# Optimization experiments

Measured on AMD Instinct MI355X. Metric: run time of the kernel, lower is better.

## Reference

```python
import jax, jax.numpy as jnp
import numpy as np

BN_EPS = 1e-5
LRELU_SLOPE = 0.2
EPS = 1e-8
K = 3


def setup_inputs() -> dict:
    key = jax.random.key(0)
    ks = jax.random.split(key, 8)
    B, Cd, Cs, M, S, N = 8, 256, 512, 4096, 1024, 4096
    return {
        "dense_data": jax.random.normal(ks[0], (B, Cd, M), dtype=jnp.float32),
        "dense_idx": jax.random.randint(ks[1], (B, M), 0, N),
        "sparse_data": jax.random.normal(ks[2], (B, Cs, S), dtype=jnp.float32),
        "sparse_idx": jax.random.randint(ks[3], (B, S), 0, N),
        "pcd": jax.random.normal(ks[4], (B, 3, N), dtype=jnp.float32),
        "conv_w": jax.random.normal(ks[5], (Cd, 3 * Cd), dtype=jnp.float32) * (1.0 / np.sqrt(3 * Cd)),
        "bn_gamma": jnp.ones((Cd,), dtype=jnp.float32),
        "bn_beta": jnp.zeros((Cd,), dtype=jnp.float32),
    }


def _knn_interpolate(dense_xyz, sparse_xyz, sparse_feats, k):
    # dense_xyz: [B,3,M], sparse_xyz: [B,3,S], sparse_feats: [B,Cs,S]
    d2 = (
        jnp.sum(dense_xyz**2, axis=1)[:, :, None]
        + jnp.sum(sparse_xyz**2, axis=1)[:, None, :]
        - 2.0 * jnp.einsum("bdm,bds->bms", dense_xyz, sparse_xyz)
    )  # [B,M,S] squared distances
    neg_d, idx = jax.lax.top_k(-d2, k)  # [B,M,K]
    d_nb = -neg_d
    w = 1.0 / (d_nb + EPS)
    w = w / jnp.sum(w, axis=-1, keepdims=True)  # [B,M,K]
    # gather neighbor features: [B,Cs,M,K]
    nb = jnp.take_along_axis(sparse_feats[:, :, None, :], idx[:, None, :, :], axis=3)
    return jnp.sum(nb * w[:, None, :, :], axis=-1)  # [B,Cs,M]


def reference(dense_data, dense_idx, sparse_data, sparse_idx, pcd, conv_w, bn_gamma, bn_beta):
    # gather xyz coords of dense / sparse points: [B,3,M], [B,3,S]
    dense_xyz = jnp.take_along_axis(pcd, dense_idx[:, None, :], axis=2)
    sparse_xyz = jnp.take_along_axis(pcd, sparse_idx[:, None, :], axis=2)
    interp = _knn_interpolate(dense_xyz, sparse_xyz, sparse_data, K)  # [B,Cs,M]
    x = jnp.concatenate([dense_data, interp], axis=1)  # [B,3*Cd,M]
    # 1x1 conv (no bias)
    y = jnp.einsum("oc,bcm->bom", conv_w, x)
    # BatchNorm1d (training mode: batch statistics over B and M, biased var)
    mu = jnp.mean(y, axis=(0, 2), keepdims=True)
    var = jnp.mean((y - mu) ** 2, axis=(0, 2), keepdims=True)
    y = (y - mu) * jax.lax.rsqrt(var + BN_EPS)
    y = y * bn_gamma[None, :, None] + bn_beta[None, :, None]
    # LeakyReLU(0.2)
    y = jnp.where(y >= 0, y, LRELU_SLOPE * y)
    return (y, dense_idx)
```

## Files before the change

kernel.cpp:

```cpp
#include <hip/hip_runtime.h>
#include <float.h>

#define DEVI __device__ __forceinline__

namespace {

constexpr int NB   = 8;
constexpr int CD   = 256;
constexpr int CS   = 512;
constexpr int MM   = 4096;
constexpr int SS   = 1024;
constexpr int NN   = 4096;
constexpr int KTOT = 768;
constexpr int OC   = 256;
constexpr float KEPS  = 1e-8f;
constexpr float BNEPS = 1e-5f;
constexpr float SLOPE = 0.2f;

constexpr size_t OFF_Z    = 0;
constexpr size_t SZ_Z     = (size_t)NB * SS * OC * 4;
constexpr size_t OFF_RAW  = OFF_Z + SZ_Z;
constexpr size_t SZ_RAW   = (size_t)NB * OC * MM * 2;
constexpr size_t OFF_IDX3 = OFF_RAW + SZ_RAW;
constexpr size_t SZ_IDX3  = (size_t)NB * MM * 3 * 4;
constexpr size_t OFF_W3   = OFF_IDX3 + SZ_IDX3;
constexpr size_t OFF_WBF  = OFF_W3 + SZ_IDX3;
constexpr size_t SZ_WBF   = (size_t)OC * KTOT * 2;
constexpr size_t OFF_PS   = OFF_WBF + SZ_WBF;
constexpr size_t SZ_PS    = (size_t)512 * OC * 4;
constexpr size_t OFF_PS2  = OFF_PS + SZ_PS;
constexpr size_t OFF_A    = OFF_PS2 + SZ_PS;
constexpr size_t OFF_B    = OFF_A + 1024;

typedef __attribute__((ext_vector_type(8))) short s16x8;
typedef __attribute__((ext_vector_type(8))) unsigned short u16x8;
typedef __attribute__((ext_vector_type(4))) float f32x4;

DEVI short f2bf(float f) {
  union { float f; unsigned u; } c; c.f = f;
  unsigned r = c.u + 0x7fffu + ((c.u >> 16) & 1u);
  return (short)(r >> 16);
}

DEVI unsigned umin_(unsigned a, unsigned b) { return a < b ? a : b; }
DEVI unsigned umax_(unsigned a, unsigned b) { return a > b ? a : b; }

__global__ __launch_bounds__(256) void k_knn(
    const int* __restrict__ didx, const int* __restrict__ sidx,
    const float* __restrict__ pcd,
    int* __restrict__ idx3, float* __restrict__ w3,
    float* __restrict__ outIdxF,
    const float* __restrict__ convw, short* __restrict__ wbf) {
  __shared__ float4   sxyz[SS];
  __shared__ unsigned pk[4][64][3];

  int blk = blockIdx.x;
  int b   = blk >> 6;
  int m0  = (blk & 63) << 6;
  int tid = threadIdx.x;
  const float* pb = pcd + (size_t)b * 3 * NN;

  for (int i = tid; i < 384; i += 256) {
    int g = blk * 384 + i;
    wbf[g] = f2bf(convw[g]);
  }

  for (int s = tid; s < SS; s += 256) {
    int si = sidx[b * SS + s];
    float x = pb[si], yy = pb[NN + si], z = pb[2 * NN + si];
    sxyz[s] = make_float4(x, yy, z, x * x + yy * yy + z * z);
  }

  int p     = tid & 63;
  int chunk = tid >> 6;
  int m     = m0 + p;
  int di    = didx[b * MM + m];
  float px = pb[di], py = pb[NN + di], pz = pb[2 * NN + di];
  float pp = px * px + py * py + pz * pz;
  float nx = -2.f * px, ny = -2.f * py, nz = -2.f * pz;

  if (chunk == 0) outIdxF[b * MM + m] = (float)di;

  __syncthreads();

  unsigned k0 = 0xFFFFFFFFu, k1 = 0xFFFFFFFFu, k2 = 0xFFFFFFFFu;
  int s0c = chunk << 8;
#pragma unroll 4
  for (int t = 0; t < 256; ++t) {
    int s = s0c + t;
    float4 c = sxyz[s];
    float d = fmaf(nx, c.x, c.w + pp);
    d = fmaf(ny, c.y, d);
    d = fmaf(nz, c.z, d);
    d = fmaxf(d, 0.f);
    unsigned key = (__float_as_uint(d) & 0xFFFFFC00u) | (unsigned)s;
    unsigned e0 = umax_(key, k0); k0 = umin_(key, k0);
    unsigned e1 = umax_(e0, k1);  k1 = umin_(e0, k1);
    k2 = umin_(e1, k2);
  }
  pk[chunk][p][0] = k0; pk[chunk][p][1] = k1; pk[chunk][p][2] = k2;
  __syncthreads();

  if (tid < 64) {
    unsigned g0 = 0xFFFFFFFFu, g1 = 0xFFFFFFFFu, g2 = 0xFFFFFFFFu;
#pragma unroll
    for (int c = 0; c < 4; ++c)
#pragma unroll
      for (int r = 0; r < 3; ++r) {
        unsigned key = pk[c][p][r];
        unsigned e0 = umax_(key, g0); g0 = umin_(key, g0);
        unsigned e1 = umax_(e0, g1);  g1 = umin_(e0, g1);
        g2 = umin_(e1, g2);
      }
    int j0 = g0 & 1023, j1 = g1 & 1023, j2 = g2 & 1023;
    float e0 = __uint_as_float(g0 & 0xFFFFFC00u);
    float e1 = __uint_as_float(g1 & 0xFFFFFC00u);
    float e2 = __uint_as_float(g2 & 0xFFFFFC00u);
    float w0 = 1.f / (e0 + KEPS), w1 = 1.f / (e1 + KEPS), w2 = 1.f / (e2 + KEPS);
    float inv = 1.f / (w0 + w1 + w2);
    int base = (b * MM + m) * 3;
    idx3[base] = j0; idx3[base + 1] = j1; idx3[base + 2] = j2;
    w3[base] = w0 * inv; w3[base + 1] = w1 * inv; w3[base + 2] = w2 * inv;
  }
}

__global__ __launch_bounds__(256) void k_gemmZ(
    const float* __restrict__ sp, const short* __restrict__ wbf,
    float* __restrict__ Z) {
  __shared__ __align__(16) short Wl[256 * 72];
  __shared__ __align__(16) short Sl[32 * 72];

  int blk = blockIdx.x;
  int st = blk & 31, b = blk >> 5;
  int s0 = st * 32;
  int tid = threadIdx.x, wv = tid >> 6, lane = tid & 63;
  int lo = lane & 15, quad = lane >> 4;

  f32x4 acc[4][2] = {};
  for (int k0 = 0; k0 < CS; k0 += 64) {
    __syncthreads();
#pragma unroll
    for (int r = 0; r < 8; ++r) {
      int lin = r * 256 + tid, row = lin >> 3, c8 = lin & 7;
      uint4 v = *(const uint4*)((const unsigned short*)wbf + (size_t)row * KTOT + CD + k0 + c8 * 8);
      *(uint4*)(&Wl[row * 72 + c8 * 8]) = v;
    }
#pragma unroll
    for (int r = 0; r < 2; ++r) {
      int lin = r * 256 + tid, cc = lin >> 3, s4 = lin & 7;
      float4 v = *(const float4*)(sp + (size_t)(b * CS + k0 + cc) * SS + s0 + s4 * 4);
      Sl[(s4 * 4 + 0) * 72 + cc] = f2bf(v.x);
      Sl[(s4 * 4 + 1) * 72 + cc] = f2bf(v.y);
      Sl[(s4 * 4 + 2) * 72 + cc] = f2bf(v.z);
      Sl[(s4 * 4 + 3) * 72 + cc] = f2bf(v.w);
    }
    __syncthreads();
    s16x8 af[2][4], bfr[2][2];
#pragma unroll
    for (int h = 0; h < 2; ++h) {
#pragma unroll
      for (int i = 0; i < 4; ++i)
        af[h][i] = *(const s16x8*)(&Wl[(wv * 64 + i * 16 + lo) * 72 + h * 32 + quad * 8]);
#pragma unroll
      for (int j = 0; j < 2; ++j)
        bfr[h][j] = *(const s16x8*)(&Sl[(j * 16 + lo) * 72 + h * 32 + quad * 8]);
    }
#pragma unroll
    for (int h = 0; h < 2; ++h)
#pragma unroll
      for (int i = 0; i < 4; ++i)
#pragma unroll
        for (int j = 0; j < 2; ++j)
          acc[i][j] = __builtin_amdgcn_mfma_f32_16x16x32_bf16(af[h][i], bfr[h][j], acc[i][j], 0, 0, 0);
  }
#pragma unroll
  for (int i = 0; i < 4; ++i)
#pragma unroll
    for (int j = 0; j < 2; ++j) {
      int s = j * 16 + lo, o = wv * 64 + i * 16 + quad * 4;
      *(f32x4*)(Z + (size_t)(b * SS + s0 + s) * OC + o) = acc[i][j];
    }
}

__global__ __launch_bounds__(256) void k_gemmDC(
    const float* __restrict__ dense, const float* __restrict__ Z,
    const int* __restrict__ idx3, const float* __restrict__ w3,
    const short* __restrict__ wbf, unsigned short* __restrict__ raw,
    float* __restrict__ ps, float* __restrict__ ps2) {
  __shared__ __align__(16) short Wl[256 * 72];
  __shared__ __align__(16) short Xl[64 * 72];
  __shared__ int   mi3[192];
  __shared__ float mw3[192];

  int blk = blockIdx.x;
  int mt = blk & 63, b = blk >> 6, m0 = mt << 6;
  int tid = threadIdx.x, wv = tid >> 6, lane = tid & 63;
  int lo = lane & 15, quad = lane >> 4;

  {
    int base = (b * MM + m0) * 3;
    for (int i = tid; i < 192; i += 256) { mi3[i] = idx3[base + i]; mw3[i] = w3[base + i]; }
  }

  f32x4 acc[4][4] = {};
  for (int k0 = 0; k0 < CD; k0 += 64) {
    __syncthreads();
#pragma unroll
    for (int r = 0; r < 8; ++r) {
      int lin = r * 256 + tid, row = lin >> 3, c8 = lin & 7;
      uint4 v = *(const uint4*)((const unsigned short*)wbf + (size_t)row * KTOT + k0 + c8 * 8);
      *(uint4*)(&Wl[row * 72 + c8 * 8]) = v;
    }
    {
      int kk4 = tid >> 4, m4 = tid & 15;
      float4 v0 = *(const float4*)(dense + (size_t)(b * CD + k0 + kk4 * 4 + 0) * MM + m0 + m4 * 4);
      float4 v1 = *(const float4*)(dense + (size_t)(b * CD + k0 + kk4 * 4 + 1) * MM + m0 + m4 * 4);
      float4 v2 = *(const float4*)(dense + (size_t)(b * CD + k0 + kk4 * 4 + 2) * MM + m0 + m4 * 4);
      float4 v3 = *(const float4*)(dense + (size_t)(b * CD + k0 + kk4 * 4 + 3) * MM + m0 + m4 * 4);
      ushort4 w;
      w.x = (unsigned short)f2bf(v0.x); w.y = (unsigned short)f2bf(v1.x);
      w.z = (unsigned short)f2bf(v2.x); w.w = (unsigned short)f2bf(v3.x);
      *(ushort4*)(&Xl[(m4 * 4 + 0) * 72 + kk4 * 4]) = w;
      w.x = (unsigned short)f2bf(v0.y); w.y = (unsigned short)f2bf(v1.y);
      w.z = (unsigned short)f2bf(v2.y); w.w = (unsigned short)f2bf(v3.y);
      *(ushort4*)(&Xl[(m4 * 4 + 1) * 72 + kk4 * 4]) = w;
      w.x = (unsigned short)f2bf(v0.z); w.y = (unsigned short)f2bf(v1.z);
      w.z = (unsigned short)f2bf(v2.z); w.w = (unsigned short)f2bf(v3.z);
      *(ushort4*)(&Xl[(m4 * 4 + 2) * 72 + kk4 * 4]) = w;
      w.x = (unsigned short)f2bf(v0.w); w.y = (unsigned short)f2bf(v1.w);
      w.z = (unsigned short)f2bf(v2.w); w.w = (unsigned short)f2bf(v3.w);
      *(ushort4*)(&Xl[(m4 * 4 + 3) * 72 + kk4 * 4]) = w;
    }
    __syncthreads();
    s16x8 af[2][4], bfr[2][4];
#pragma unroll
    for (int h = 0; h < 2; ++h) {
#pragma unroll
      for (int i = 0; i < 4; ++i)
        af[h][i] = *(const s16x8*)(&Wl[(wv * 64 + i * 16 + lo) * 72 + h * 32 + quad * 8]);
#pragma unroll
      for (int j = 0; j < 4; ++j)
        bfr[h][j] = *(const s16x8*)(&Xl[(j * 16 + lo) * 72 + h * 32 + quad * 8]);
    }
#pragma unroll
    for (int h = 0; h < 2; ++h)
#pragma unroll
      for (int i = 0; i < 4; ++i)
#pragma unroll
        for (int j = 0; j < 4; ++j)
          acc[i][j] = __builtin_amdgcn_mfma_f32_16x16x32_bf16(af[h][i], bfr[h][j], acc[i][j], 0, 0, 0);
  }

  float* P = (float*)Wl;
  const float* Zb = Z + (size_t)b * SS * OC;
  unsigned short* rb = raw + (size_t)b * OC * MM;
  float ss[4][4] = {}, s2s[4][4] = {};
  __syncthreads();

#pragma unroll
  for (int h = 0; h < 2; ++h) {
#pragma unroll 4
    for (int ml = 0; ml < 32; ++ml) {
      int mg = (h * 32 + ml) * 3;
      float p = mw3[mg + 0] * Zb[(size_t)mi3[mg + 0] * OC + tid]
              + mw3[mg + 1] * Zb[(size_t)mi3[mg + 1] * OC + tid]
              + mw3[mg + 2] * Zb[(size_t)mi3[mg + 2] * OC + tid];
      P[ml * 260 + tid] = p;
    }
    __syncthreads();
#pragma unroll
    for (int i = 0; i < 4; ++i)
#pragma unroll
      for (int jj = 0; jj < 2; ++jj) {
        int j = h * 2 + jj, ml = jj * 16 + lo;
        int o = wv * 64 + i * 16 + quad * 4;
        f32x4 p = *(const f32x4*)(&P[ml * 260 + o]);
        f32x4 v = acc[i][j] + p;
        unsigned short* dst = rb + (size_t)o * MM + m0 + j * 16 + lo;
#pragma unroll
        for (int r = 0; r < 4; ++r) {
          float vv = v[r];
          dst[(size_t)r * MM] = (unsigned short)f2bf(vv);
          ss[i][r] += vv; s2s[i][r] += vv * vv;
        }
      }
    __syncthreads();
  }

#pragma unroll
  for (int i = 0; i < 4; ++i)
#pragma unroll
    for (int r = 0; r < 4; ++r) {
      float a = ss[i][r], q = s2s[i][r];
      for (int off = 1; off < 16; off <<= 1) { a += __shfl_xor(a, off); q += __shfl_xor(q, off); }
      ss[i][r] = a; s2s[i][r] = q;
    }
  if (lo == 0) {
#pragma unroll
    for (int i = 0; i < 4; ++i)
#pragma unroll
      for (int r = 0; r < 4; ++r) {
        int o = wv * 64 + i * 16 + quad * 4 + r;
        ps[(size_t)blk * OC + o]  = ss[i][r];
        ps2[(size_t)blk * OC + o] = s2s[i][r];
      }
  }
}

__global__ void k_finalize(const float* __restrict__ ps, const float* __restrict__ ps2,
                           const float* __restrict__ gamma, const float* __restrict__ beta,
                           float* __restrict__ sA, float* __restrict__ sB) {
  __shared__ float red[512];
  int blk = blockIdx.x;
  int tid = threadIdx.x;
  int ch = tid & 31, sl = tid >> 5;
  int o = blk * 32 + ch;
  float s = 0.f, s2 = 0.f;
#pragma unroll 4
  for (int j = 0; j < 64; ++j) {
    int k = sl * 64 + j;
    s  += ps[(size_t)k * OC + o];
    s2 += ps2[(size_t)k * OC + o];
  }
  red[sl * 32 + ch] = s;
  red[256 + sl * 32 + ch] = s2;
  __syncthreads();
  if (tid < 32) {
    float S = 0.f, S2 = 0.f;
#pragma unroll
    for (int t = 0; t < 8; ++t) { S += red[t * 32 + tid]; S2 += red[256 + t * 32 + tid]; }
    int oo = blk * 32 + tid;
    float mn = S / (float)(NB * MM);
    float vr = S2 / (float)(NB * MM) - mn * mn;
    float a  = rsqrtf(vr + BNEPS) * gamma[oo];
    sA[oo] = a;
    sB[oo] = beta[oo] - mn * a;
  }
}

__global__ void k_norm(const unsigned short* __restrict__ raw, float* __restrict__ y,
                       const float* __restrict__ sA, const float* __restrict__ sB) {
  int i = blockIdx.x * 256 + threadIdx.x;
  int o = (i >> 9) & 255;
  float a = sA[o], be = sB[o];
  u16x8 v = ((const u16x8*)raw)[i];
  float out[8];
#pragma unroll
  for (int r = 0; r < 8; ++r) {
    union { unsigned u; float f; } c; c.u = ((unsigned)v[r]) << 16;
    float t = c.f * a + be;
    out[r] = t >= 0.f ? t : SLOPE * t;
  }
  float4* dst = (float4*)(y + (size_t)i * 8);
  dst[0] = make_float4(out[0], out[1], out[2], out[3]);
  dst[1] = make_float4(out[4], out[5], out[6], out[7]);
}

}

extern "C" void kernel_launch(void* const* d_in, const int* in_sizes, int n_in,
                              void* d_out, int out_size, void* d_ws, size_t ws_size,
                              hipStream_t stream) {
  const float* dense = (const float*)d_in[0];
  const int*   didx  = (const int*)d_in[1];
  const float* sp    = (const float*)d_in[2];
  const int*   sidx  = (const int*)d_in[3];
  const float* pcd   = (const float*)d_in[4];
  const float* convw = (const float*)d_in[5];
  const float* gamma = (const float*)d_in[6];
  const float* beta  = (const float*)d_in[7];

  float* y = (float*)d_out;
  float* outIdxF = y + (size_t)NB * OC * MM;

  char* ws = (char*)d_ws;
  float*          Z    = (float*)(ws + OFF_Z);
  unsigned short* raw  = (unsigned short*)(ws + OFF_RAW);
  int*            idx3 = (int*)(ws + OFF_IDX3);
  float*          w3   = (float*)(ws + OFF_W3);
  short*          wbf  = (short*)(ws + OFF_WBF);
  float*          ps   = (float*)(ws + OFF_PS);
  float*          ps2  = (float*)(ws + OFF_PS2);
  float*          sA   = (float*)(ws + OFF_A);
  float*          sB   = (float*)(ws + OFF_B);

  k_knn     <<<NB * (MM / 64), 256, 0, stream>>>(didx, sidx, pcd, idx3, w3, outIdxF, convw, wbf);
  k_gemmZ   <<<NB * (SS / 32), 256, 0, stream>>>(sp, wbf, Z);
  k_gemmDC  <<<NB * (MM / 64), 256, 0, stream>>>(dense, Z, idx3, w3, wbf, raw, ps, ps2);
  k_finalize<<<8, 256, 0, stream>>>(ps, ps2, gamma, beta, sA, sB);
  k_norm    <<<(NB * OC * MM / 8) / 256, 256, 0, stream>>>(raw, y, sA, sB);
}
```

Measured before the change: 163.3 us.

## Fuse BN finalize into normalize kernel and process two query points per KNN thread

The BN statistics finalize kernel is removed: partial sums are now stored channel-major, and each normalize block (one per batch/channel row) reduces the 512 partials for its channel before applying scale, shift and LeakyReLU. This drops one kernel launch and the tiny 8-block finalize stage, but repeats the channel reduction across all 8 batches. Separately, the KNN kernel now handles 128 query points per block, two per thread. Each shared-memory read of sparse xyz is reused for two distance computations, and half as many blocks reload the sparse coordinates.

Result: no change. 163.9 us (+0.4%).

```diff
diff --git a/kernel.cpp b/kernel.cpp
--- a/kernel.cpp
+++ b/kernel.cpp
@@ -29,8 +29,6 @@
 constexpr size_t OFF_PS   = OFF_WBF + SZ_WBF;
 constexpr size_t SZ_PS    = (size_t)512 * OC * 4;
 constexpr size_t OFF_PS2  = OFF_PS + SZ_PS;
-constexpr size_t OFF_A    = OFF_PS2 + SZ_PS;
-constexpr size_t OFF_B    = OFF_A + 1024;
 
 typedef __attribute__((ext_vector_type(8))) short s16x8;
 typedef __attribute__((ext_vector_type(8))) unsigned short u16x8;
@@ -52,16 +50,16 @@
     float* __restrict__ outIdxF,
     const float* __restrict__ convw, short* __restrict__ wbf) {
   __shared__ float4   sxyz[SS];
-  __shared__ unsigned pk[4][64][3];
+  __shared__ unsigned pk[4][128][3];
 
   int blk = blockIdx.x;
-  int b   = blk >> 6;
-  int m0  = (blk & 63) << 6;
+  int b   = blk >> 5;
+  int m0  = (blk & 31) << 7;
   int tid = threadIdx.x;
   const float* pb = pcd + (size_t)b * 3 * NN;
 
-  for (int i = tid; i < 384; i += 256) {
-    int g = blk * 384 + i;
+  for (int i = tid; i < 768; i += 256) {
+    int g = blk * 768 + i;
     wbf[g] = f2bf(convw[g]);
   }
 
@@ -73,41 +71,57 @@
 
   int p     = tid & 63;
   int chunk = tid >> 6;
-  int m     = m0 + p;
-  int di    = didx[b * MM + m];
-  float px = pb[di], py = pb[NN + di], pz = pb[2 * NN + di];
-  float pp = px * px + py * py + pz * pz;
-  float nx = -2.f * px, ny = -2.f * py, nz = -2.f * pz;
-
-  if (chunk == 0) outIdxF[b * MM + m] = (float)di;
+  int mA    = m0 + p, mB = m0 + p + 64;
+  int diA = didx[b * MM + mA], diB = didx[b * MM + mB];
+  float pxA = pb[diA], pyA = pb[NN + diA], pzA = pb[2 * NN + diA];
+  float pxB = pb[diB], pyB = pb[NN + diB], pzB = pb[2 * NN + diB];
+  float ppA = pxA * pxA + pyA * pyA + pzA * pzA;
+  float ppB = pxB * pxB + pyB * pyB + pzB * pzB;
+  float nxA = -2.f * pxA, nyA = -2.f * pyA, nzA = -2.f * pzA;
+  float nxB = -2.f * pxB, nyB = -2.f * pyB, nzB = -2.f * pzB;
+
+  if (chunk == 0) {
+    outIdxF[b * MM + mA] = (float)diA;
+    outIdxF[b * MM + mB] = (float)diB;
+  }
 
   __syncthreads();
 
-  unsigned k0 = 0xFFFFFFFFu, k1 = 0xFFFFFFFFu, k2 = 0xFFFFFFFFu;
+  unsigned a0 = 0xFFFFFFFFu, a1 = 0xFFFFFFFFu, a2 = 0xFFFFFFFFu;
+  unsigned c0 = 0xFFFFFFFFu, c1 = 0xFFFFFFFFu, c2 = 0xFFFFFFFFu;
   int s0c = chunk << 8;
 #pragma unroll 4
   for (int t = 0; t < 256; ++t) {
     int s = s0c + t;
     float4 c = sxyz[s];
-    float d = fmaf(nx, c.x, c.w + pp);
-    d = fmaf(ny, c.y, d);
-    d = fmaf(nz, c.z, d);
-    d = fmaxf(d, 0.f);
-    unsigned key = (__float_as_uint(d) & 0xFFFFFC00u) | (unsigned)s;
-    unsigned e0 = umax_(key, k0); k0 = umin_(key, k0);
-    unsigned e1 = umax_(e0, k1);  k1 = umin_(e0, k1);
-    k2 = umin_(e1, k2);
-  }
-  pk[chunk][p][0] = k0; pk[chunk][p][1] = k1; pk[chunk][p][2] = k2;
+    float dA = fmaf(nxA, c.x, c.w + ppA);
+    dA = fmaf(nyA, c.y, dA);
+    dA = fmaf(nzA, c.z, dA);
+    dA = fmaxf(dA, 0.f);
+    unsigned keyA = (__float_as_uint(dA) & 0xFFFFFC00u) | (unsigned)s;
+    unsigned eA0 = umax_(keyA, a0); a0 = umin_(keyA, a0);
+    unsigned eA1 = umax_(eA0, a1);  a1 = umin_(eA0, a1);
+    a2 = umin_(eA1, a2);
+    float dB = fmaf(nxB, c.x, c.w + ppB);
+    dB = fmaf(nyB, c.y, dB);
+    dB = fmaf(nzB, c.z, dB);
+    dB = fmaxf(dB, 0.f);
+    unsigned keyB = (__float_as_uint(dB) & 0xFFFFFC00u) | (unsigned)s;
+    unsigned eB0 = umax_(keyB, c0); c0 = umin_(keyB, c0);
+    unsigned eB1 = umax_(eB0, c1);  c1 = umin_(eB0, c1);
+    c2 = umin_(eB1, c2);
+  }
+  pk[chunk][p][0] = a0;      pk[chunk][p][1] = a1;      pk[chunk][p][2] = a2;
+  pk[chunk][p + 64][0] = c0; pk[chunk][p + 64][1] = c1; pk[chunk][p + 64][2] = c2;
   __syncthreads();
 
-  if (tid < 64) {
+  if (tid < 128) {
     unsigned g0 = 0xFFFFFFFFu, g1 = 0xFFFFFFFFu, g2 = 0xFFFFFFFFu;
 #pragma unroll
     for (int c = 0; c < 4; ++c)
 #pragma unroll
       for (int r = 0; r < 3; ++r) {
-        unsigned key = pk[c][p][r];
+        unsigned key = pk[c][tid][r];
         unsigned e0 = umax_(key, g0); g0 = umin_(key, g0);
         unsigned e1 = umax_(e0, g1);  g1 = umin_(e0, g1);
         g2 = umin_(e1, g2);
@@ -118,7 +132,7 @@
     float e2 = __uint_as_float(g2 & 0xFFFFFC00u);
     float w0 = 1.f / (e0 + KEPS), w1 = 1.f / (e1 + KEPS), w2 = 1.f / (e2 + KEPS);
     float inv = 1.f / (w0 + w1 + w2);
-    int base = (b * MM + m) * 3;
+    int base = (b * MM + m0 + tid) * 3;
     idx3[base] = j0; idx3[base + 1] = j1; idx3[base + 2] = j2;
     w3[base] = w0 * inv; w3[base + 1] = w1 * inv; w3[base + 2] = w2 * inv;
   }
@@ -301,59 +315,57 @@
 #pragma unroll
       for (int r = 0; r < 4; ++r) {
         int o = wv * 64 + i * 16 + quad * 4 + r;
-        ps[(size_t)blk * OC + o]  = ss[i][r];
-        ps2[(size_t)blk * OC + o] = s2s[i][r];
+        ps[(size_t)o * 512 + blk]  = ss[i][r];
+        ps2[(size_t)o * 512 + blk] = s2s[i][r];
       }
   }
 }
 
-__global__ void k_finalize(const float* __restrict__ ps, const float* __restrict__ ps2,
-                           const float* __restrict__ gamma, const float* __restrict__ beta,
-                           float* __restrict__ sA, float* __restrict__ sB) {
-  __shared__ float red[512];
-  int blk = blockIdx.x;
-  int tid = threadIdx.x;
-  int ch = tid & 31, sl = tid >> 5;
-  int o = blk * 32 + ch;
-  float s = 0.f, s2 = 0.f;
-#pragma unroll 4
-  for (int j = 0; j < 64; ++j) {
-    int k = sl * 64 + j;
-    s  += ps[(size_t)k * OC + o];
-    s2 += ps2[(size_t)k * OC + o];
-  }
-  red[sl * 32 + ch] = s;
-  red[256 + sl * 32 + ch] = s2;
+__global__ __launch_bounds__(256) void k_norm(
+    const unsigned short* __restrict__ raw, float* __restrict__ y,
+    const float* __restrict__ ps, const float* __restrict__ ps2,
+    const float* __restrict__ gamma, const float* __restrict__ beta) {
+  __shared__ float rw[8];
+  __shared__ float sAB[2];
+  int bo = blockIdx.x;
+  int b = bo >> 8, o = bo & 255;
+  int tid = threadIdx.x, wv = tid >> 6, lane = tid & 63;
+
+  float s  = ps[(size_t)o * 512 + tid]  + ps[(size_t)o * 512 + 256 + tid];
+  float s2 = ps2[(size_t)o * 512 + tid] + ps2[(size_t)o * 512 + 256 + tid];
+#pragma unroll
+  for (int off = 32; off; off >>= 1) { s += __shfl_down(s, off); s2 += __shfl_down(s2, off); }
+  if (lane == 0) { rw[wv] = s; rw[4 + wv] = s2; }
   __syncthreads();
-  if (tid < 32) {
-    float S = 0.f, S2 = 0.f;
-#pragma unroll
-    for (int t = 0; t < 8; ++t) { S += red[t * 32 + tid]; S2 += red[256 + t * 32 + tid]; }
-    int oo = blk * 32 + tid;
+  if (tid == 0) {
+    float S = rw[0] + rw[1] + rw[2] + rw[3];
+    float S2 = rw[4] + rw[5] + rw[6] + rw[7];
     float mn = S / (float)(NB * MM);
     float vr = S2 / (float)(NB * MM) - mn * mn;
-    float a  = rsqrtf(vr + BNEPS) * gamma[oo];
-    sA[oo] = a;
-    sB[oo] = beta[oo] - mn * a;
-  }
-}
-
-__global__ void k_norm(const unsigned short* __restrict__ raw, float* __restrict__ y,
-                       const float* __restrict__ sA, const float* __restrict__ sB) {
-  int i = blockIdx.x * 256 + threadIdx.x;
-  int o = (i >> 9) & 255;
-  float a = sA[o], be = sB[o];
-  u16x8 v = ((const u16x8*)raw)[i];
-  float out[8];
-#pragma unroll
-  for (int r = 0; r < 8; ++r) {
-    union { unsigned u; float f; } c; c.u = ((unsigned)v[r]) << 16;
-    float t = c.f * a + be;
-    out[r] = t >= 0.f ? t : SLOPE * t;
-  }
-  float4* dst = (float4*)(y + (size_t)i * 8);
-  dst[0] = make_float4(out[0], out[1], out[2], out[3]);
-  dst[1] = make_float4(out[4], out[5], out[6], out[7]);
+    float a  = rsqrtf(vr + BNEPS) * gamma[o];
+    sAB[0] = a;
+    sAB[1] = beta[o] - mn * a;
+  }
+  __syncthreads();
+  float a = sAB[0], be = sAB[1];
+
+  const unsigned short* row = raw + (size_t)(b * OC + o) * MM;
+  float* dst = y + (size_t)(b * OC + o) * MM;
+#pragma unroll
+  for (int u = 0; u < 2; ++u) {
+    int i = tid * 2 + u;
+    u16x8 v = ((const u16x8*)row)[i];
+    float out[8];
+#pragma unroll
+    for (int r = 0; r < 8; ++r) {
+      union { unsigned u; float f; } c; c.u = ((unsigned)v[r]) << 16;
+      float t = c.f * a + be;
+      out[r] = t >= 0.f ? t : SLOPE * t;
+    }
+    float4* d4 = (float4*)(dst + (size_t)i * 8);
+    d4[0] = make_float4(out[0], out[1], out[2], out[3]);
+    d4[1] = make_float4(out[4], out[5], out[6], out[7]);
+  }
 }
 
 }
@@ -381,12 +393,9 @@
   short*          wbf  = (short*)(ws + OFF_WBF);
   float*          ps   = (float*)(ws + OFF_PS);
   float*          ps2  = (float*)(ws + OFF_PS2);
-  float*          sA   = (float*)(ws + OFF_A);
-  float*          sB   = (float*)(ws + OFF_B);
-
-  k_knn     <<<NB * (MM / 64), 256, 0, stream>>>(didx, sidx, pcd, idx3, w3, outIdxF, convw, wbf);
-  k_gemmZ   <<<NB * (SS / 32), 256, 0, stream>>>(sp, wbf, Z);
-  k_gemmDC  <<<NB * (MM / 64), 256, 0, stream>>>(dense, Z, idx3, w3, wbf, raw, ps, ps2);
-  k_finalize<<<8, 256, 0, stream>>>(ps, ps2, gamma, beta, sA, sB);
-  k_norm    <<<(NB * OC * MM / 8) / 256, 256, 0, stream>>>(raw, y, sA, sB);
-}
+
+  k_knn   <<<NB * (MM / 128), 256, 0, stream>>>(didx, sidx, pcd, idx3, w3, outIdxF, convw, wbf);
+  k_gemmZ <<<NB * (SS / 32), 256, 0, stream>>>(sp, wbf, Z);
+  k_gemmDC<<<NB * (MM / 64), 256, 0, stream>>>(dense, Z, idx3, w3, wbf, raw, ps, ps2);
+  k_norm  <<<NB * OC, 256, 0, stream>>>(raw, y, ps, ps2, gamma, beta);
+}
```
